# Kernel tuning notes

Hardware: AMD Instinct MI355X
Metric: run time of the kernel (lower is better)

Reference implementation:

```python
import jax, jax.numpy as jnp
import numpy as np

N_NODES = 50000
N_EDGES = 800000
F_IN = 64
HID = 64
N_CLASSES = 10


def setup_inputs() -> dict:
    key = jax.random.key(0)
    ks = jax.random.split(key, 16)
    features = jax.random.normal(ks[0], (N_NODES, F_IN), dtype=jnp.float32)
    edge_indicies = jax.random.randint(ks[1], (2, N_EDGES), 0, N_NODES, dtype=jnp.int64)
    s = 1.0 / np.sqrt(HID)
    params = {}
    # three GINConv MLPs: Linear(in,64) -> ReLU -> Linear(64,64)
    for i in range(3):
        d_in = F_IN if i == 0 else HID
        si = 1.0 / np.sqrt(d_in)
        params[f"W1_{i}"] = jax.random.uniform(ks[2 + 4 * i], (d_in, HID), jnp.float32, -si, si)
        params[f"b1_{i}"] = jax.random.uniform(ks[3 + 4 * i], (HID,), jnp.float32, -si, si)
        params[f"W2_{i}"] = jax.random.uniform(ks[4 + 4 * i], (HID, HID), jnp.float32, -s, s)
        params[f"b2_{i}"] = jax.random.uniform(ks[5 + 4 * i], (HID,), jnp.float32, -s, s)
    params["W_lin"] = jax.random.uniform(ks[14], (HID, N_CLASSES), jnp.float32, -s, s)
    params["b_lin"] = jax.random.uniform(ks[15], (N_CLASSES,), jnp.float32, -s, s)
    return {"features": features, "edge_indicies": edge_indicies, **params}


def _gin_conv(x, src, dst, W1, b1, W2, b2):
    # aggregate: sum_{j in N(i)} x_j  (messages flow src -> dst), eps = 0
    agg = jax.ops.segment_sum(x[src], dst, num_segments=N_NODES)
    h = agg + x  # (1 + eps) * x + aggregate, eps=0
    # MLP: Linear -> ReLU -> Linear
    return jax.nn.relu(h @ W1 + b1) @ W2 + b2


def reference(features, edge_indicies,
              W1_0, b1_0, W2_0, b2_0,
              W1_1, b1_1, W2_1, b2_1,
              W1_2, b1_2, W2_2, b2_2,
              W_lin, b_lin):
    src, dst = edge_indicies[0], edge_indicies[1]
    x = jax.nn.relu(_gin_conv(features, src, dst, W1_0, b1_0, W2_0, b2_0))
    x = jax.nn.relu(_gin_conv(x, src, dst, W1_1, b1_1, W2_1, b2_1))
    x = jax.nn.relu(_gin_conv(x, src, dst, W1_2, b1_2, W2_2, b2_2))
    return x @ W_lin + b_lin
```

## Files before the change

### kernel.cpp

```cpp
#include <hip/hip_runtime.h>
#include <hip/hip_bf16.h>

#define FDIM 64
#define BNODES 64
#define CHUNK 8192
#define HP 72
#define GCAP 768

typedef short bf16x8 __attribute__((ext_vector_type(8)));
typedef float f32x4 __attribute__((ext_vector_type(4)));

__device__ __forceinline__ unsigned short f2bf(float f) {
    unsigned int u = __float_as_uint(f);
    unsigned int r = (u + 0x7fffu + ((u >> 16) & 1u)) >> 16;
    return (unsigned short)r;
}
__device__ __forceinline__ float bflo(unsigned int p) { return __uint_as_float(p << 16); }
__device__ __forceinline__ float bfhi(unsigned int p) { return __uint_as_float(p & 0xffff0000u); }

__global__ __launch_bounds__(256) void cast_bf16(const float* __restrict__ x,
                                                 unsigned short* __restrict__ xb, int n4) {
    int i = blockIdx.x * blockDim.x + threadIdx.x;
    if (i < n4) {
        float4 v = ((const float4*)x)[i];
        uint2 o;
        o.x = (unsigned int)f2bf(v.x) | ((unsigned int)f2bf(v.y) << 16);
        o.y = (unsigned int)f2bf(v.z) | ((unsigned int)f2bf(v.w) << 16);
        ((uint2*)xb)[i] = o;
    }
}

__global__ __launch_bounds__(256) void bucket_hist(const int* __restrict__ dst,
                                                   int* __restrict__ hist,
                                                   int n_edges, int nbuck) {
    __shared__ int lh[1024];
    int chunk = blockIdx.x;
    for (int i = threadIdx.x; i < nbuck; i += 256) lh[i] = 0;
    __syncthreads();
    int beg = chunk * CHUNK;
    int end = min(beg + CHUNK, n_edges);
    for (int e = beg + threadIdx.x; e < end; e += 256)
        atomicAdd(&lh[dst[e] >> 6], 1);
    __syncthreads();
    for (int i = threadIdx.x; i < nbuck; i += 256)
        hist[(size_t)chunk * nbuck + i] = lh[i];
}

__global__ __launch_bounds__(256) void scan_chunks(const int* __restrict__ hist,
                                                   int* __restrict__ chunk_off,
                                                   int* __restrict__ bucket_total,
                                                   int nchunks, int nbuck) {
    __shared__ int s[256];
    int b = blockIdx.x;
    int t = threadIdx.x;
    int v = (t < nchunks) ? hist[(size_t)t * nbuck + b] : 0;
    s[t] = v;
    __syncthreads();
    for (int off = 1; off < 256; off <<= 1) {
        int u = (t >= off) ? s[t - off] : 0;
        __syncthreads();
        s[t] += u;
        __syncthreads();
    }
    if (t < nchunks) chunk_off[(size_t)t * nbuck + b] = s[t] - v;
    if (t == 255) bucket_total[b] = s[255];
}

__global__ __launch_bounds__(1024) void scan_buckets(const int* __restrict__ bucket_total,
                                                     int* __restrict__ bucket_start,
                                                     int* __restrict__ row_ptr,
                                                     int nbuck, int n_nodes, int n_edges) {
    __shared__ int s[1024];
    int t = threadIdx.x;
    int v = (t < nbuck) ? bucket_total[t] : 0;
    s[t] = v;
    __syncthreads();
    for (int off = 1; off < 1024; off <<= 1) {
        int u = (t >= off) ? s[t - off] : 0;
        __syncthreads();
        s[t] += u;
        __syncthreads();
    }
    if (t < nbuck) bucket_start[t] = s[t] - v;
    if (t == 0) { bucket_start[nbuck] = n_edges; row_ptr[n_nodes] = n_edges; }
}

__global__ __launch_bounds__(256) void bucket_fill(const int* __restrict__ src,
                                                   const int* __restrict__ dst,
                                                   const int* __restrict__ bucket_start,
                                                   const int* __restrict__ chunk_off,
                                                   unsigned int* __restrict__ packed,
                                                   int n_edges, int nbuck) {
    __shared__ int cur[1024];
    int chunk = blockIdx.x;
    for (int i = threadIdx.x; i < nbuck; i += 256)
        cur[i] = bucket_start[i] + chunk_off[(size_t)chunk * nbuck + i];
    __syncthreads();
    int beg = chunk * CHUNK;
    int end = min(beg + CHUNK, n_edges);
    for (int e = beg + threadIdx.x; e < end; e += 256) {
        int d = dst[e];
        int b = d >> 6;
        int pos = atomicAdd(&cur[b], 1);
        packed[pos] = (unsigned int)src[e] | ((unsigned int)(d & 63) << 16);
    }
}

__global__ __launch_bounds__(256) void sort_bucket(const unsigned int* __restrict__ packed,
                                                   const int* __restrict__ bucket_start,
                                                   int* __restrict__ src_sorted,
                                                   int* __restrict__ row_ptr, int n_nodes) {
    __shared__ int cnt[BNODES];
    __shared__ int cur[BNODES];
    int b = blockIdx.x;
    int beg = bucket_start[b], end = bucket_start[b + 1];
    if (threadIdx.x < BNODES) cnt[threadIdx.x] = 0;
    __syncthreads();
    for (int e = beg + threadIdx.x; e < end; e += 256)
        atomicAdd(&cnt[packed[e] >> 16], 1);
    __syncthreads();
    if (threadIdx.x < 64) {
        int v = cnt[threadIdx.x];
        int inc = v;
#pragma unroll
        for (int off = 1; off < 64; off <<= 1) {
            int u = __shfl_up(inc, off, 64);
            if (threadIdx.x >= off) inc += u;
        }
        cur[threadIdx.x] = beg + inc - v;
        int node = b * BNODES + threadIdx.x;
        if (node < n_nodes) row_ptr[node] = beg + inc - v;
    }
    __syncthreads();
    for (int e = beg + threadIdx.x; e < end; e += 256) {
        unsigned int p = packed[e];
        int pos = atomicAdd(&cur[p >> 16], 1);
        src_sorted[pos] = (int)(p & 0xFFFFu);
    }
}

__global__ __launch_bounds__(256) void gather_bf16(const unsigned short* __restrict__ xb,
                                                   const int* __restrict__ row_ptr,
                                                   const int* __restrict__ src_sorted,
                                                   unsigned short* __restrict__ hb,
                                                   int n_nodes) {
    __shared__ int sidx[GCAP];
    int base = blockIdx.x * 16;
    int ebeg = row_ptr[base];
    int eend = row_ptr[min(base + 16, n_nodes)];
    int total = eend - ebeg;
    int cnt = min(total, GCAP);
    for (int i = threadIdx.x; i < cnt; i += 256) sidx[i] = src_sorted[ebeg + i];
    __syncthreads();

    int t = threadIdx.x;
    int node = base + (t >> 4);
    if (node >= n_nodes) return;
    int c = (t & 15) * 4;
    int dbeg = row_ptr[node] - ebeg;
    int dend = row_ptr[node + 1] - ebeg;

    float4 acc;
    {
        uint2 v = *(const uint2*)(xb + (size_t)node * FDIM + c);
        acc.x = bflo(v.x); acc.y = bfhi(v.x);
        acc.z = bflo(v.y); acc.w = bfhi(v.y);
    }

    if (total <= GCAP) {
        int e = dbeg;
        for (; e + 7 < dend; e += 8) {
            int s[8];
#pragma unroll
            for (int j = 0; j < 8; j++) s[j] = sidx[e + j];
            uint2 v[8];
#pragma unroll
            for (int j = 0; j < 8; j++) v[j] = *(const uint2*)(xb + (size_t)s[j] * FDIM + c);
#pragma unroll
            for (int j = 0; j < 8; j++) {
                acc.x += bflo(v[j].x); acc.y += bfhi(v[j].x);
                acc.z += bflo(v[j].y); acc.w += bfhi(v[j].y);
            }
        }
        if (e + 3 < dend) {
            int s[4];
#pragma unroll
            for (int j = 0; j < 4; j++) s[j] = sidx[e + j];
            uint2 v[4];
#pragma unroll
            for (int j = 0; j < 4; j++) v[j] = *(const uint2*)(xb + (size_t)s[j] * FDIM + c);
#pragma unroll
            for (int j = 0; j < 4; j++) {
                acc.x += bflo(v[j].x); acc.y += bfhi(v[j].x);
                acc.z += bflo(v[j].y); acc.w += bfhi(v[j].y);
            }
            e += 4;
        }
        for (; e < dend; e++) {
            uint2 v = *(const uint2*)(xb + (size_t)sidx[e] * FDIM + c);
            acc.x += bflo(v.x); acc.y += bfhi(v.x);
            acc.z += bflo(v.y); acc.w += bfhi(v.y);
        }
    } else {
        for (int e = dbeg; e < dend; e++) {
            int si = (e < cnt) ? sidx[e] : src_sorted[ebeg + e];
            uint2 v = *(const uint2*)(xb + (size_t)si * FDIM + c);
            acc.x += bflo(v.x); acc.y += bfhi(v.x);
            acc.z += bflo(v.y); acc.w += bfhi(v.y);
        }
    }

    uint2 p;
    p.x = (unsigned int)f2bf(acc.x) | ((unsigned int)f2bf(acc.y) << 16);
    p.y = (unsigned int)f2bf(acc.z) | ((unsigned int)f2bf(acc.w) << 16);
    *(uint2*)(hb + (size_t)node * FDIM + c) = p;
}

__global__ __launch_bounds__(256) void mlp_mfma(const unsigned short* __restrict__ xb,
        const float* __restrict__ W1, const float* __restrict__ b1,
        const float* __restrict__ W2, const float* __restrict__ b2,
        const float* __restrict__ Wl, const float* __restrict__ bl,
        unsigned short* __restrict__ y, float* __restrict__ out,
        int n_nodes, int do_final) {
    __shared__ unsigned short sH[64 * HP];
    __shared__ unsigned short sW1t[64 * HP];
    __shared__ unsigned short sW2t[64 * HP];
    __shared__ float sb1[FDIM], sb2[FDIM];
    __shared__ float sWl[FDIM * 10];
    __shared__ float sbl[16];

    int tid = threadIdx.x;
    int base = blockIdx.x * 64;

#pragma unroll
    for (int p = 0; p < 4; p++) {
        int idx = tid + p * 256;
        int k = idx >> 4;
        int n0 = (idx & 15) * 4;
        float4 v1 = ((const float4*)W1)[idx];
        float4 v2 = ((const float4*)W2)[idx];
        sW1t[(n0 + 0) * HP + k] = f2bf(v1.x);
        sW1t[(n0 + 1) * HP + k] = f2bf(v1.y);
        sW1t[(n0 + 2) * HP + k] = f2bf(v1.z);
        sW1t[(n0 + 3) * HP + k] = f2bf(v1.w);
        sW2t[(n0 + 0) * HP + k] = f2bf(v2.x);
        sW2t[(n0 + 1) * HP + k] = f2bf(v2.y);
        sW2t[(n0 + 2) * HP + k] = f2bf(v2.z);
        sW2t[(n0 + 3) * HP + k] = f2bf(v2.w);
    }
    if (tid < FDIM) { sb1[tid] = b1[tid]; sb2[tid] = b2[tid]; }
    if (do_final) {
        for (int i = tid; i < FDIM * 10; i += 256) sWl[i] = Wl[i];
        if (tid < 10) sbl[tid] = bl[tid];
    }
#pragma unroll
    for (int p = 0; p < 2; p++) {
        int idx = tid + p * 256;
        int r = idx >> 3, q = idx & 7;
        uint4 v = make_uint4(0u, 0u, 0u, 0u);
        if (base + r < n_nodes) v = *(const uint4*)(xb + (size_t)(base + r) * FDIM + q * 8);
        *(uint4*)(&sH[r * HP + q * 8]) = v;
    }
    __syncthreads();

    int w = tid >> 6;
    int lane = tid & 63;
    int qd = lane >> 4;
    int m = lane & 15;
    int arow = (w * 16 + m) * HP;

    f32x4 acc[4];

    {
        bf16x8 a0 = *(bf16x8*)(&sH[arow + qd * 8]);
        bf16x8 a1 = *(bf16x8*)(&sH[arow + 32 + qd * 8]);
#pragma unroll
        for (int t = 0; t < 4; t++) {
            float bias = sb1[t * 16 + m];
            acc[t] = (f32x4){bias, bias, bias, bias};
            bf16x8 bA = *(bf16x8*)(&sW1t[(t * 16 + m) * HP + qd * 8]);
            bf16x8 bB = *(bf16x8*)(&sW1t[(t * 16 + m) * HP + 32 + qd * 8]);
            acc[t] = __builtin_amdgcn_mfma_f32_16x16x32_bf16(a0, bA, acc[t], 0, 0, 0);
            acc[t] = __builtin_amdgcn_mfma_f32_16x16x32_bf16(a1, bB, acc[t], 0, 0, 0);
        }
#pragma unroll
        for (int t = 0; t < 4; t++)
#pragma unroll
            for (int r = 0; r < 4; r++)
                sH[(w * 16 + qd * 4 + r) * HP + t * 16 + m] = f2bf(fmaxf(acc[t][r], 0.f));
    }

    {
        bf16x8 a0 = *(bf16x8*)(&sH[arow + qd * 8]);
        bf16x8 a1 = *(bf16x8*)(&sH[arow + 32 + qd * 8]);
#pragma unroll
        for (int t = 0; t < 4; t++) {
            float bias = sb2[t * 16 + m];
            acc[t] = (f32x4){bias, bias, bias, bias};
            bf16x8 bA = *(bf16x8*)(&sW2t[(t * 16 + m) * HP + qd * 8]);
            bf16x8 bB = *(bf16x8*)(&sW2t[(t * 16 + m) * HP + 32 + qd * 8]);
            acc[t] = __builtin_amdgcn_mfma_f32_16x16x32_bf16(a0, bA, acc[t], 0, 0, 0);
            acc[t] = __builtin_amdgcn_mfma_f32_16x16x32_bf16(a1, bB, acc[t], 0, 0, 0);
        }
#pragma unroll
        for (int t = 0; t < 4; t++)
#pragma unroll
            for (int r = 0; r < 4; r++)
                sH[(w * 16 + qd * 4 + r) * HP + t * 16 + m] = f2bf(fmaxf(acc[t][r], 0.f));
    }
    __syncthreads();

    if (!do_final) {
#pragma unroll
        for (int p = 0; p < 2; p++) {
            int idx = tid + p * 256;
            int r = idx >> 3, q = idx & 7;
            if (base + r < n_nodes)
                *(uint4*)(y + (size_t)(base + r) * FDIM + q * 8) = *(uint4*)(&sH[r * HP + q * 8]);
        }
    } else {
        for (int i = tid; i < 64 * 10; i += 256) {
            int nl = i / 10, cc = i % 10;
            int node = base + nl;
            if (node < n_nodes) {
                float s = sbl[cc];
#pragma unroll
                for (int k0 = 0; k0 < FDIM; k0 += 4) {
                    uint2 hp = *(uint2*)(&sH[nl * HP + k0]);
                    s += bflo(hp.x) * sWl[(k0 + 0) * 10 + cc] + bfhi(hp.x) * sWl[(k0 + 1) * 10 + cc]
                       + bflo(hp.y) * sWl[(k0 + 2) * 10 + cc] + bfhi(hp.y) * sWl[(k0 + 3) * 10 + cc];
                }
                out[(size_t)node * 10 + cc] = s;
            }
        }
    }
}

extern "C" void kernel_launch(void* const* d_in, const int* in_sizes, int n_in,
                              void* d_out, int out_size, void* d_ws, size_t ws_size,
                              hipStream_t stream) {
    const float* features = (const float*)d_in[0];
    const int* edges = (const int*)d_in[1];
    int n_nodes = in_sizes[0] / FDIM;
    int n_edges = in_sizes[1] / 2;
    const int* src = edges;
    const int* dst = edges + n_edges;

    int nbuck = (n_nodes + BNODES - 1) / BNODES;
    int nchunks = (n_edges + CHUNK - 1) / CHUNK;

    int* hist = (int*)d_ws;
    int* chunk_off = hist + (size_t)nchunks * nbuck;
    int* bucket_total = chunk_off + (size_t)nchunks * nbuck;
    int* bucket_start = bucket_total + nbuck;
    int* row_ptr = bucket_start + nbuck + 1;
    unsigned int* packed = (unsigned int*)(row_ptr + n_nodes + 1);
    int* src_sorted = (int*)(packed + n_edges);
    size_t int_elems = 2 * (size_t)nchunks * nbuck + 2 * (size_t)nbuck + 2
                       + (size_t)n_nodes + 2 * (size_t)n_edges;
    int_elems = (int_elems + 3) & ~(size_t)3;
    size_t buf_elems = (size_t)n_nodes * FDIM;
    unsigned short* hb  = (unsigned short*)((int*)d_ws + int_elems);
    unsigned short* xb0 = hb + buf_elems;
    unsigned short* yA  = xb0 + buf_elems;
    unsigned short* yB  = yA + buf_elems;

    dim3 bs(256);
    dim3 gs_cast(((int)(buf_elems / 4) + 255) / 256);
    dim3 gs_gather((n_nodes + 15) / 16);
    dim3 gs_tile((n_nodes + 63) / 64);

    cast_bf16<<<gs_cast, bs, 0, stream>>>(features, xb0, (int)(buf_elems / 4));

    bucket_hist<<<nchunks, 256, 0, stream>>>(dst, hist, n_edges, nbuck);
    scan_chunks<<<nbuck, 256, 0, stream>>>(hist, chunk_off, bucket_total, nchunks, nbuck);
    scan_buckets<<<1, 1024, 0, stream>>>(bucket_total, bucket_start, row_ptr, nbuck, n_nodes, n_edges);
    bucket_fill<<<nchunks, 256, 0, stream>>>(src, dst, bucket_start, chunk_off, packed, n_edges, nbuck);
    sort_bucket<<<nbuck, 256, 0, stream>>>(packed, bucket_start, src_sorted, row_ptr, n_nodes);

    const float* Wl = (const float*)d_in[14];
    const float* bl = (const float*)d_in[15];
    const unsigned short* x_cur = xb0;
    unsigned short* outs[3] = {yA, yB, yA};
    for (int conv = 0; conv < 3; conv++) {
        const float* W1 = (const float*)d_in[2 + 4 * conv];
        const float* b1 = (const float*)d_in[3 + 4 * conv];
        const float* W2 = (const float*)d_in[4 + 4 * conv];
        const float* b2 = (const float*)d_in[5 + 4 * conv];
        int fin = (conv == 2) ? 1 : 0;

        gather_bf16<<<gs_gather, bs, 0, stream>>>(x_cur, row_ptr, src_sorted, hb, n_nodes);
        mlp_mfma<<<gs_tile, bs, 0, stream>>>(hb, W1, b1, W2, b2, Wl, bl,
                                             outs[conv], (float*)d_out, n_nodes, fin);
        x_cur = outs[conv];
    }
}
```

Measured before the change: 223.7 us.

## Widen gather loads to 16B per lane and precompute transposed bf16 weights

The gather kernel now gives each node 8 lanes, each loading 16 bytes per neighbour row instead of 8 bytes, and each block handles 32 nodes with a larger shared index cache. The overflow path is restructured so the cached part is unrolled and only the tail reads src_sorted from global memory. A new prep_weights kernel converts and transposes the six MLP weight matrices to bf16 once, so every mlp_mfma block copies ready-made tiles instead of converting fp32 weights itself. This adds one small kernel launch and extra workspace, and it leaves fewer lanes in flight per neighbour load in the gather.

```diff
diff --git a/kernel.cpp b/kernel.cpp
--- a/kernel.cpp
+++ b/kernel.cpp
@@ -5,7 +5,7 @@
 #define BNODES 64
 #define CHUNK 8192
 #define HP 72
-#define GCAP 768
+#define GCAP 2048
 
 typedef short bf16x8 __attribute__((ext_vector_type(8)));
 typedef float f32x4 __attribute__((ext_vector_type(4)));
@@ -27,6 +27,44 @@
         o.x = (unsigned int)f2bf(v.x) | ((unsigned int)f2bf(v.y) << 16);
         o.y = (unsigned int)f2bf(v.z) | ((unsigned int)f2bf(v.w) << 16);
         ((uint2*)xb)[i] = o;
+    }
+}
+
+__global__ __launch_bounds__(256) void prep_weights(const float* __restrict__ W10,
+                                                    const float* __restrict__ W20,
+                                                    const float* __restrict__ W11,
+                                                    const float* __restrict__ W21,
+                                                    const float* __restrict__ W12,
+                                                    const float* __restrict__ W22,
+                                                    unsigned short* __restrict__ wt) {
+    __shared__ unsigned short s[64 * 64];
+    const float* W;
+    switch (blockIdx.x) {
+        case 0: W = W10; break;
+        case 1: W = W20; break;
+        case 2: W = W11; break;
+        case 3: W = W21; break;
+        case 4: W = W12; break;
+        default: W = W22; break;
+    }
+    int tid = threadIdx.x;
+#pragma unroll
+    for (int p = 0; p < 4; p++) {
+        int idx = tid + p * 256;
+        int k = idx >> 4;
+        int n0 = (idx & 15) * 4;
+        float4 v = ((const float4*)W)[idx];
+        s[(n0 + 0) * 64 + k] = f2bf(v.x);
+        s[(n0 + 1) * 64 + k] = f2bf(v.y);
+        s[(n0 + 2) * 64 + k] = f2bf(v.z);
+        s[(n0 + 3) * 64 + k] = f2bf(v.w);
+    }
+    __syncthreads();
+    uint4* o = (uint4*)(wt + (size_t)blockIdx.x * 4096);
+#pragma unroll
+    for (int p = 0; p < 2; p++) {
+        int idx = tid + p * 256;
+        o[idx] = ((uint4*)s)[idx];
     }
 }
 
@@ -145,80 +183,89 @@
                                                    unsigned short* __restrict__ hb,
                                                    int n_nodes) {
     __shared__ int sidx[GCAP];
-    int base = blockIdx.x * 16;
+    int base = blockIdx.x * 32;
     int ebeg = row_ptr[base];
-    int eend = row_ptr[min(base + 16, n_nodes)];
+    int eend = row_ptr[min(base + 32, n_nodes)];
     int total = eend - ebeg;
     int cnt = min(total, GCAP);
     for (int i = threadIdx.x; i < cnt; i += 256) sidx[i] = src_sorted[ebeg + i];
     __syncthreads();
 
     int t = threadIdx.x;
-    int node = base + (t >> 4);
+    int node = base + (t >> 3);
     if (node >= n_nodes) return;
-    int c = (t & 15) * 4;
+    int c = (t & 7) * 8;
     int dbeg = row_ptr[node] - ebeg;
     int dend = row_ptr[node + 1] - ebeg;
-
-    float4 acc;
+    int dmid = (total <= GCAP) ? dend : min(dend, cnt);
+
+    float acc[8];
     {
-        uint2 v = *(const uint2*)(xb + (size_t)node * FDIM + c);
-        acc.x = bflo(v.x); acc.y = bfhi(v.x);
-        acc.z = bflo(v.y); acc.w = bfhi(v.y);
-    }
-
-    if (total <= GCAP) {
-        int e = dbeg;
-        for (; e + 7 < dend; e += 8) {
-            int s[8];
-#pragma unroll
-            for (int j = 0; j < 8; j++) s[j] = sidx[e + j];
-            uint2 v[8];
-#pragma unroll
-            for (int j = 0; j < 8; j++) v[j] = *(const uint2*)(xb + (size_t)s[j] * FDIM + c);
-#pragma unroll
-            for (int j = 0; j < 8; j++) {
-                acc.x += bflo(v[j].x); acc.y += bfhi(v[j].x);
-                acc.z += bflo(v[j].y); acc.w += bfhi(v[j].y);
-            }
-        }
-        if (e + 3 < dend) {
-            int s[4];
-#pragma unroll
-            for (int j = 0; j < 4; j++) s[j] = sidx[e + j];
-            uint2 v[4];
-#pragma unroll
-            for (int j = 0; j < 4; j++) v[j] = *(const uint2*)(xb + (size_t)s[j] * FDIM + c);
-#pragma unroll
-            for (int j = 0; j < 4; j++) {
-                acc.x += bflo(v[j].x); acc.y += bfhi(v[j].x);
-                acc.z += bflo(v[j].y); acc.w += bfhi(v[j].y);
-            }
-            e += 4;
-        }
-        for (; e < dend; e++) {
-            uint2 v = *(const uint2*)(xb + (size_t)sidx[e] * FDIM + c);
-            acc.x += bflo(v.x); acc.y += bfhi(v.x);
-            acc.z += bflo(v.y); acc.w += bfhi(v.y);
-        }
-    } else {
-        for (int e = dbeg; e < dend; e++) {
-            int si = (e < cnt) ? sidx[e] : src_sorted[ebeg + e];
-            uint2 v = *(const uint2*)(xb + (size_t)si * FDIM + c);
-            acc.x += bflo(v.x); acc.y += bfhi(v.x);
-            acc.z += bflo(v.y); acc.w += bfhi(v.y);
-        }
-    }
-
-    uint2 p;
-    p.x = (unsigned int)f2bf(acc.x) | ((unsigned int)f2bf(acc.y) << 16);
-    p.y = (unsigned int)f2bf(acc.z) | ((unsigned int)f2bf(acc.w) << 16);
-    *(uint2*)(hb + (size_t)node * FDIM + c) = p;
+        uint4 v = *(const uint4*)(xb + (size_t)node * FDIM + c);
+        acc[0] = bflo(v.x); acc[1] = bfhi(v.x);
+        acc[2] = bflo(v.y); acc[3] = bfhi(v.y);
+        acc[4] = bflo(v.z); acc[5] = bfhi(v.z);
+        acc[6] = bflo(v.w); acc[7] = bfhi(v.w);
+    }
+
+    int e = dbeg;
+    for (; e + 7 < dmid; e += 8) {
+        int s[8];
+#pragma unroll
+        for (int j = 0; j < 8; j++) s[j] = sidx[e + j];
+        uint4 v[8];
+#pragma unroll
+        for (int j = 0; j < 8; j++) v[j] = *(const uint4*)(xb + (size_t)s[j] * FDIM + c);
+#pragma unroll
+        for (int j = 0; j < 8; j++) {
+            acc[0] += bflo(v[j].x); acc[1] += bfhi(v[j].x);
+            acc[2] += bflo(v[j].y); acc[3] += bfhi(v[j].y);
+            acc[4] += bflo(v[j].z); acc[5] += bfhi(v[j].z);
+            acc[6] += bflo(v[j].w); acc[7] += bfhi(v[j].w);
+        }
+    }
+    if (e + 3 < dmid) {
+        int s[4];
+#pragma unroll
+        for (int j = 0; j < 4; j++) s[j] = sidx[e + j];
+        uint4 v[4];
+#pragma unroll
+        for (int j = 0; j < 4; j++) v[j] = *(const uint4*)(xb + (size_t)s[j] * FDIM + c);
+#pragma unroll
+        for (int j = 0; j < 4; j++) {
+            acc[0] += bflo(v[j].x); acc[1] += bfhi(v[j].x);
+            acc[2] += bflo(v[j].y); acc[3] += bfhi(v[j].y);
+            acc[4] += bflo(v[j].z); acc[5] += bfhi(v[j].z);
+            acc[6] += bflo(v[j].w); acc[7] += bfhi(v[j].w);
+        }
+        e += 4;
+    }
+    for (; e < dmid; e++) {
+        uint4 v = *(const uint4*)(xb + (size_t)sidx[e] * FDIM + c);
+        acc[0] += bflo(v.x); acc[1] += bfhi(v.x);
+        acc[2] += bflo(v.y); acc[3] += bfhi(v.y);
+        acc[4] += bflo(v.z); acc[5] += bfhi(v.z);
+        acc[6] += bflo(v.w); acc[7] += bfhi(v.w);
+    }
+    for (; e < dend; e++) {
+        uint4 v = *(const uint4*)(xb + (size_t)src_sorted[ebeg + e] * FDIM + c);
+        acc[0] += bflo(v.x); acc[1] += bfhi(v.x);
+        acc[2] += bflo(v.y); acc[3] += bfhi(v.y);
+        acc[4] += bflo(v.z); acc[5] += bfhi(v.z);
+        acc[6] += bflo(v.w); acc[7] += bfhi(v.w);
+    }
+
+    uint4 p;
+    p.x = (unsigned int)f2bf(acc[0]) | ((unsigned int)f2bf(acc[1]) << 16);
+    p.y = (unsigned int)f2bf(acc[2]) | ((unsigned int)f2bf(acc[3]) << 16);
+    p.z = (unsigned int)f2bf(acc[4]) | ((unsigned int)f2bf(acc[5]) << 16);
+    p.w = (unsigned int)f2bf(acc[6]) | ((unsigned int)f2bf(acc[7]) << 16);
+    *(uint4*)(hb + (size_t)node * FDIM + c) = p;
 }
 
 __global__ __launch_bounds__(256) void mlp_mfma(const unsigned short* __restrict__ xb,
-        const float* __restrict__ W1, const float* __restrict__ b1,
-        const float* __restrict__ W2, const float* __restrict__ b2,
+        const unsigned short* __restrict__ wt1, const float* __restrict__ b1,
+        const unsigned short* __restrict__ wt2, const float* __restrict__ b2,
         const float* __restrict__ Wl, const float* __restrict__ bl,
         unsigned short* __restrict__ y, float* __restrict__ out,
         int n_nodes, int do_final) {
@@ -232,21 +279,16 @@
     int tid = threadIdx.x;
     int base = blockIdx.x * 64;
 
-#pragma unroll
-    for (int p = 0; p < 4; p++) {
-        int idx = tid + p * 256;
-        int k = idx >> 4;
-        int n0 = (idx & 15) * 4;
-        float4 v1 = ((const float4*)W1)[idx];
-        float4 v2 = ((const float4*)W2)[idx];
-        sW1t[(n0 + 0) * HP + k] = f2bf(v1.x);
-        sW1t[(n0 + 1) * HP + k] = f2bf(v1.y);
-        sW1t[(n0 + 2) * HP + k] = f2bf(v1.z);
-        sW1t[(n0 + 3) * HP + k] = f2bf(v1.w);
-        sW2t[(n0 + 0) * HP + k] = f2bf(v2.x);
-        sW2t[(n0 + 1) * HP + k] = f2bf(v2.y);
-        sW2t[(n0 + 2) * HP + k] = f2bf(v2.z);
-        sW2t[(n0 + 3) * HP + k] = f2bf(v2.w);
+    {
+        const uint4* w1g = (const uint4*)wt1;
+        const uint4* w2g = (const uint4*)wt2;
+#pragma unroll
+        for (int p = 0; p < 2; p++) {
+            int idx = tid + p * 256;
+            int r = idx >> 3, q = idx & 7;
+            *(uint4*)(&sW1t[r * HP + q * 8]) = w1g[idx];
+            *(uint4*)(&sW2t[r * HP + q * 8]) = w2g[idx];
+        }
     }
     if (tid < FDIM) { sb1[tid] = b1[tid]; sb2[tid] = b2[tid]; }
     if (do_final) {
@@ -364,13 +406,17 @@
     unsigned short* xb0 = hb + buf_elems;
     unsigned short* yA  = xb0 + buf_elems;
     unsigned short* yB  = yA + buf_elems;
+    unsigned short* wt  = yB + buf_elems;
 
     dim3 bs(256);
     dim3 gs_cast(((int)(buf_elems / 4) + 255) / 256);
-    dim3 gs_gather((n_nodes + 15) / 16);
+    dim3 gs_gather((n_nodes + 31) / 32);
     dim3 gs_tile((n_nodes + 63) / 64);
 
     cast_bf16<<<gs_cast, bs, 0, stream>>>(features, xb0, (int)(buf_elems / 4));
+    prep_weights<<<6, bs, 0, stream>>>((const float*)d_in[2], (const float*)d_in[4],
+                                       (const float*)d_in[6], (const float*)d_in[8],
+                                       (const float*)d_in[10], (const float*)d_in[12], wt);
 
     bucket_hist<<<nchunks, 256, 0, stream>>>(dst, hist, n_edges, nbuck);
     scan_chunks<<<nbuck, 256, 0, stream>>>(hist, chunk_off, bucket_total, nchunks, nbuck);
@@ -383,14 +429,14 @@
     const unsigned short* x_cur = xb0;
     unsigned short* outs[3] = {yA, yB, yA};
     for (int conv = 0; conv < 3; conv++) {
-        const float* W1 = (const float*)d_in[2 + 4 * conv];
         const float* b1 = (const float*)d_in[3 + 4 * conv];
-        const float* W2 = (const float*)d_in[4 + 4 * conv];
         const float* b2 = (const float*)d_in[5 + 4 * conv];
+        const unsigned short* wt1 = wt + (size_t)(2 * conv) * 4096;
+        const unsigned short* wt2 = wt + (size_t)(2 * conv + 1) * 4096;
         int fin = (conv == 2) ? 1 : 0;
 
         gather_bf16<<<gs_gather, bs, 0, stream>>>(x_cur, row_ptr, src_sorted, hb, n_nodes);
-        mlp_mfma<<<gs_tile, bs, 0, stream>>>(hb, W1, b1, W2, b2, Wl, bl,
+        mlp_mfma<<<gs_tile, bs, 0, stream>>>(hb, wt1, b1, wt2, b2, Wl, bl,
                                              outs[conv], (float*)d_out, n_nodes, fin);
         x_cur = outs[conv];
     }
```

New measurement: 217.0 us. 3.0% less time.
